# Kernel optimization log

Measured on AMD Instinct MI355X. Metric: run time of the kernel, lower is better.

## Reference

```python
import jax, jax.numpy as jnp
import numpy as np
from jax import lax

B, C, H, W, K = 32, 128, 56, 56, 5
CR = C // 4          # reduced channels in weight-gen MLP
CE = 4 * C           # expanded channels
EPS = 1e-6


def setup_inputs() -> dict:
    key = jax.random.key(0)
    ks = jax.random.split(key, 8)
    s = lambda fan: 1.0 / np.sqrt(fan)
    return {
        "x": jax.random.normal(ks[0], (B, C, H, W), jnp.float32),
        "w_fc1": jax.random.normal(ks[1], (CR, C), jnp.float32) * s(C),
        "ln1_w": jnp.ones((CR,), jnp.float32),
        "ln1_b": jnp.zeros((CR,), jnp.float32),
        "w_fc2": jax.random.normal(ks[2], (C * K * K, CR), jnp.float32) * s(CR),
        "ln2_w": jnp.ones((C,), jnp.float32),
        "ln2_b": jnp.zeros((C,), jnp.float32),
        "w_expand": jax.random.normal(ks[3], (CE, C), jnp.float32) * s(C),
        "w_shrink": jax.random.normal(ks[4], (C, CE), jnp.float32) * s(CE),
        "grn_gamma": jax.random.normal(ks[5], (CE,), jnp.float32) * 0.1,
        "grn_beta": jax.random.normal(ks[6], (CE,), jnp.float32) * 0.1,
    }


def _ln(v, w, b, axis):
    u = v.mean(axis, keepdims=True)
    s2 = jnp.square(v - u).mean(axis, keepdims=True)
    return (v - u) * lax.rsqrt(s2 + EPS) * w + b


def reference(x, w_fc1, ln1_w, ln1_b, w_fc2, ln2_w, ln2_b, w_expand, w_shrink,
              grn_gamma, grn_beta):
    b, c, h, w = x.shape
    # ---- dynamic weight generation: pool -> fc1 -> LN -> fc2 ----
    pooled = x.mean((2, 3))                                  # [B, C]
    hdn = pooled @ w_fc1.T                                   # [B, CR]
    hdn = _ln(hdn, ln1_w, ln1_b, axis=-1)                    # channels_first LN over CR
    dyn = hdn @ w_fc2.T                                      # [B, C*K*K]
    dyn_w = dyn.reshape(b * c, 1, K, K)                      # per-sample depthwise kernels
    # ---- per-sample dynamic depthwise conv (groups = B*C) ----
    pad = K // 2
    out = lax.conv_general_dilated(
        x.reshape(1, b * c, h, w), dyn_w,
        window_strides=(1, 1), padding=[(pad, pad), (pad, pad)],
        dimension_numbers=("NCHW", "OIHW", "NCHW"),
        feature_group_count=b * c,
    ).reshape(b, c, h, w)
    # ---- LN (channels_first) over channel dim ----
    u = out.mean(1, keepdims=True)
    s2 = jnp.square(out - u).mean(1, keepdims=True)
    out = (out - u) * lax.rsqrt(s2 + EPS)
    out = ln2_w[None, :, None, None] * out + ln2_b[None, :, None, None]
    # ---- expand 1x1 -> GELU -> GRN -> shrink 1x1 ----
    out = jnp.einsum("bchw,oc->bohw", out, w_expand)         # [B, 4C, H, W]
    out = jax.nn.gelu(out, approximate=False)
    gx = jnp.sqrt(jnp.sum(jnp.square(out), axis=(2, 3), keepdims=True))  # [B,4C,1,1]
    nx = gx / (gx.mean(1, keepdims=True) + EPS)
    g = grn_gamma[None, :, None, None]
    bt = grn_beta[None, :, None, None]
    out = g * (out * nx) + bt + out
    out = jnp.einsum("bohw,co->bchw", out, w_shrink)         # [B, C, H, W]
    return out + x
```

## Files before the change

kernel.cpp:

```cpp
#include <hip/hip_runtime.h>
#include <hip/hip_bf16.h>

#define B_   32
#define C_   128
#define H_   56
#define W_   56
#define HW_  (H_*W_)
#define BHW_ (B_*HW_)
#define K5_  5
#define KK_  25
#define CR_  32
#define CE_  512
#define EPS_ 1e-6f

typedef __hip_bfloat16 bf16;
typedef __attribute__((ext_vector_type(8))) short short8;
typedef __attribute__((ext_vector_type(4))) float f32x4;


__device__ __forceinline__ float wave_reduce_sum(float v) {
#pragma unroll
  for (int off = 32; off > 0; off >>= 1) v += __shfl_down(v, off, 64);
  return v;
}
__device__ __forceinline__ float bf2f(unsigned short u) {
  return __uint_as_float(((unsigned)u) << 16);
}
__device__ __forceinline__ unsigned short f2bf_bits(float f) {
  bf16 h = __float2bfloat16(f);
  unsigned short u;
  __builtin_memcpy(&u, &h, 2);
  return u;
}
__device__ __forceinline__ float fast_gelu(float v) {
  float t = __expf(-1.702f * v);
  return v * __builtin_amdgcn_rcpf(1.0f + t);
}
__device__ __forceinline__ void glds16(const void* g, void* l) {
  __builtin_amdgcn_global_load_lds(
      (const __attribute__((address_space(1))) unsigned int*)g,
      (__attribute__((address_space(3))) unsigned int*)l, 16, 0, 0);
}

__global__ __launch_bounds__(256) void prep_kernel(const float* __restrict__ we,
                                                   const float* __restrict__ ws,
                                                   const float* __restrict__ beta,
                                                   bf16* __restrict__ weB,
                                                   bf16* __restrict__ wsB,
                                                   float* __restrict__ gx2,
                                                   float* __restrict__ sb) {
  if (blockIdx.x < 576) {
    int i = blockIdx.x * 256 + threadIdx.x;
    if (i < CE_ * C_)          weB[i] = __float2bfloat16(we[i]);
    else if (i < 2 * CE_ * C_) wsB[i - CE_ * C_] = __float2bfloat16(ws[i - CE_ * C_]);
    else                       gx2[i - 2 * CE_ * C_] = 0.f;
  } else {
    int c = blockIdx.x - 576;
    const float* wp = ws + (size_t)c * CE_;
    float acc = 0.f;
    for (int o = threadIdx.x; o < CE_; o += 256) acc += wp[o] * beta[o];
    acc = wave_reduce_sum(acc);
    __shared__ float red[4];
    int lane = threadIdx.x & 63, wid = threadIdx.x >> 6;
    if (lane == 0) red[wid] = acc;
    __syncthreads();
    if (threadIdx.x == 0) sb[c] = red[0] + red[1] + red[2] + red[3];
  }
}

__global__ __launch_bounds__(256) void pool_kernel(const float* __restrict__ x,
                                                   float* __restrict__ pooled) {
  int bc = blockIdx.x;
  const float4* xp4 = reinterpret_cast<const float4*>(x + (size_t)bc * HW_);
  float s = 0.f;
  for (int i = threadIdx.x; i < 784; i += 256) {
    float4 v = xp4[i];
    s += (v.x + v.y) + (v.z + v.w);
  }
  s = wave_reduce_sum(s);
  __shared__ float red[4];
  int lane = threadIdx.x & 63, wid = threadIdx.x >> 6;
  if (lane == 0) red[wid] = s;
  __syncthreads();
  if (threadIdx.x == 0) pooled[bc] = (red[0] + red[1] + red[2] + red[3]) * (1.0f / HW_);
}

__global__ __launch_bounds__(256) void fc_kernel(const float* __restrict__ pooled,
                                                 const float* __restrict__ w_fc1,
                                                 const float* __restrict__ ln1_w,
                                                 const float* __restrict__ ln1_b,
                                                 const float* __restrict__ w_fc2,
                                                 float* __restrict__ dyn) {
  int b = blockIdx.x;
  int tid = threadIdx.x;
  __shared__ float sp[C_];
  __shared__ float sh[CR_];
  __shared__ float shn[CR_];
  __shared__ float stats[2];
  if (tid < C_) sp[tid] = pooled[b * C_ + tid];
  __syncthreads();
  if (tid < CR_) {
    float acc = 0.f;
    const float* wr = w_fc1 + tid * C_;
#pragma unroll 4
    for (int c = 0; c < C_; ++c) acc += sp[c] * wr[c];
    sh[tid] = acc;
  }
  __syncthreads();
  if (tid == 0) {
    float u = 0.f;
    for (int j = 0; j < CR_; ++j) u += sh[j];
    u *= (1.0f / CR_);
    float v = 0.f;
    for (int j = 0; j < CR_; ++j) { float d = sh[j] - u; v += d * d; }
    v *= (1.0f / CR_);
    stats[0] = u;
    stats[1] = rsqrtf(v + EPS_);
  }
  __syncthreads();
  if (tid < CR_) shn[tid] = (sh[tid] - stats[0]) * stats[1] * ln1_w[tid] + ln1_b[tid];
  __syncthreads();
  for (int i = tid; i < C_ * KK_; i += 256) {
    const float* wr = w_fc2 + i * CR_;
    float acc = 0.f;
#pragma unroll
    for (int j = 0; j < CR_; ++j) acc += shn[j] * wr[j];
    dyn[b * (C_ * KK_) + i] = acc;
  }
}

__global__ __launch_bounds__(256) void conv_kernel(const float* __restrict__ x,
                                                   const float* __restrict__ dyn,
                                                   bf16* __restrict__ z) {
  int bc = blockIdx.x;
  int b = bc >> 7;
  int c = bc & 127;
  int tid = threadIdx.x;
  __shared__ float xs[(H_ + 4) * 64];
  __shared__ float wks[KK_];
  {
    int r = tid >> 6;
    int rr = (r < 2) ? r : (56 + r);
    xs[rr * 64 + (tid & 63)] = 0.f;
  }
  if (tid < 224) {
    int r = tid >> 2, q = tid & 3;
    int col = (q < 2) ? q : (56 + q);
    xs[(r + 2) * 64 + col] = 0.f;
  }
  if (tid < KK_) wks[tid] = dyn[b * (C_ * KK_) + c * KK_ + tid];
  const float4* xp4 = reinterpret_cast<const float4*>(x + (size_t)bc * HW_);
  for (int i = tid; i < 784; i += 256) {
    float4 v = xp4[i];
    int h = i / 14, w4 = (i % 14) * 4;
    float* dst = &xs[(h + 2) * 64 + 2 + w4];
    dst[0] = v.x; dst[1] = v.y; dst[2] = v.z; dst[3] = v.w;
  }
  __syncthreads();
  float wr[KK_];
#pragma unroll
  for (int j = 0; j < KK_; ++j) wr[j] = wks[j];
  for (int g = tid; g < 784; g += 256) {
    int h = g / 14;
    int w4 = (g % 14) * 4;
    float a0 = 0.f, a1 = 0.f, a2 = 0.f, a3 = 0.f;
#pragma unroll
    for (int dh = 0; dh < K5_; ++dh) {
      const float* row = &xs[(h + dh) * 64 + w4];
      float4 va = *reinterpret_cast<const float4*>(row);
      float4 vb = *reinterpret_cast<const float4*>(row + 4);
      float v0 = va.x, v1 = va.y, v2 = va.z, v3 = va.w;
      float v4 = vb.x, v5 = vb.y, v6 = vb.z, v7 = vb.w;
      float u0 = wr[dh * 5 + 0], u1 = wr[dh * 5 + 1], u2 = wr[dh * 5 + 2];
      float u3 = wr[dh * 5 + 3], u4 = wr[dh * 5 + 4];
      a0 += v0 * u0 + v1 * u1 + v2 * u2 + v3 * u3 + v4 * u4;
      a1 += v1 * u0 + v2 * u1 + v3 * u2 + v4 * u3 + v5 * u4;
      a2 += v2 * u0 + v3 * u1 + v4 * u2 + v5 * u3 + v6 * u4;
      a3 += v3 * u0 + v4 * u1 + v5 * u2 + v6 * u3 + v7 * u4;
    }
    size_t base = (size_t)bc * HW_ + h * W_ + w4;
    ushort4 pk = make_ushort4(f2bf_bits(a0), f2bf_bits(a1), f2bf_bits(a2), f2bf_bits(a3));
    *reinterpret_cast<ushort4*>(reinterpret_cast<unsigned short*>(z) + base) = pk;
  }
}

__global__ __launch_bounds__(256) void ln_kernel(const bf16* __restrict__ z,
                                                 const float* __restrict__ ln2_w,
                                                 const float* __restrict__ ln2_b,
                                                 bf16* __restrict__ yT) {
  int hw0 = blockIdx.x * 64;
  int b = blockIdx.y;
  int tid = threadIdx.x;
  int wq = tid & 63;
  int cq = tid >> 6;
  __shared__ unsigned short zt[C_][64];
  __shared__ unsigned short yt[64][136];
  __shared__ float redS[4][64];
  __shared__ float redQ[4][64];
  __shared__ float meanArr[64];
  __shared__ float invArr[64];
  const unsigned short* zp = reinterpret_cast<const unsigned short*>(z);
#pragma unroll
  for (int i = 0; i < 4; ++i) {
    int t = tid + 256 * i;
    int c = t >> 3, ch = t & 7;
    int4 v = *reinterpret_cast<const int4*>(zp + ((size_t)(b * C_ + c)) * HW_ + hw0 + ch * 8);
    *reinterpret_cast<int4*>(&zt[c][ch * 8]) = v;
  }
  __syncthreads();
  float s = 0.f, q = 0.f;
#pragma unroll 4
  for (int k = 0; k < 32; ++k) {
    float v = bf2f(zt[cq * 32 + k][wq]);
    s += v;
    q += v * v;
  }
  redS[cq][wq] = s;
  redQ[cq][wq] = q;
  __syncthreads();
  if (cq == 0) {
    float ss = redS[0][wq] + redS[1][wq] + redS[2][wq] + redS[3][wq];
    float qq = redQ[0][wq] + redQ[1][wq] + redQ[2][wq] + redQ[3][wq];
    float m = ss * (1.0f / C_);
    float var = qq * (1.0f / C_) - m * m;
    meanArr[wq] = m;
    invArr[wq] = rsqrtf(fmaxf(var, 0.f) + EPS_);
  }
  __syncthreads();
  float m = meanArr[wq], iv = invArr[wq];
#pragma unroll
  for (int g = 0; g < 4; ++g) {
    unsigned short pk[8];
#pragma unroll
    for (int i = 0; i < 8; ++i) {
      int c = cq * 32 + g * 8 + i;
      float v = bf2f(zt[c][wq]);
      pk[i] = f2bf_bits((v - m) * iv * ln2_w[c] + ln2_b[c]);
    }
    int4 t;
    __builtin_memcpy(&t, pk, 16);
    *reinterpret_cast<int4*>(&yt[wq][cq * 32 + g * 8]) = t;
  }
  __syncthreads();
  unsigned short* yp = reinterpret_cast<unsigned short*>(yT);
#pragma unroll
  for (int i = 0; i < 4; ++i) {
    int t = tid + 256 * i;
    int row = t >> 4, ch = t & 15;
    int4 v = *reinterpret_cast<const int4*>(&yt[row][ch * 8]);
    *reinterpret_cast<int4*>(yp + ((size_t)(b * HW_ + hw0 + row)) * C_ + ch * 8) = v;
  }
}

__global__ __launch_bounds__(256, 4) void gx2_pass(const bf16* __restrict__ yT,
                                                   const bf16* __restrict__ weB,
                                                   float* __restrict__ gx2) {
  int j0 = blockIdx.x * 128;
  int o0 = blockIdx.y * 128;
  int tid = threadIdx.x;
  int lane = tid & 63, wid = tid >> 6;
  int wm = wid >> 1, wn = wid & 1;
  int quad = lane >> 4, l15 = lane & 15;
  __shared__ __align__(16) char smem[32768];
  const short* yS = reinterpret_cast<const short*>(yT);
  const short* weS = reinterpret_cast<const short*>(weB);
  int sr = (wid * 2) * 16 + (lane >> 2);
  int scp = lane & 3;
  auto STAGE = [&](int bs, int k0) {
#pragma unroll
    for (int i = 0; i < 2; ++i) {
      int seg = wid * 2 + i;
      int r = sr + i * 16;
      int c = scp ^ ((r >> 1) & 3);
      char* base = smem + bs * 16384 + seg * 1024;
      glds16(yS + (size_t)(j0 + r) * C_ + k0 + c * 8, base);
      glds16(weS + (size_t)(o0 + r) * C_ + k0 + c * 8, base + 8192);
    }
  };
  f32x4 acc[4][4] = {};
  STAGE(0, 0);
  __syncthreads();
#pragma unroll
  for (int t = 0; t < 4; ++t) {
    if (t < 3) STAGE((t + 1) & 1, (t + 1) * 32);
    const char* ba = smem + (t & 1) * 16384;
    int sx = (quad ^ ((l15 >> 1) & 3)) * 16;
    short8 a[4], bfr[4];
#pragma unroll
    for (int mf = 0; mf < 4; ++mf)
      a[mf] = *reinterpret_cast<const short8*>(ba + (wm * 64 + mf * 16 + l15) * 64 + sx);
#pragma unroll
    for (int nf = 0; nf < 4; ++nf)
      bfr[nf] = *reinterpret_cast<const short8*>(ba + 8192 + (wn * 64 + nf * 16 + l15) * 64 + sx);
#pragma unroll
    for (int mf = 0; mf < 4; ++mf)
#pragma unroll
      for (int nf = 0; nf < 4; ++nf)
        acc[mf][nf] = __builtin_amdgcn_mfma_f32_16x16x32_bf16(a[mf], bfr[nf], acc[mf][nf], 0, 0, 0);
    __syncthreads();
  }
#pragma unroll
  for (int mf = 0; mf < 4; ++mf) {
    int jm = j0 + wm * 64 + mf * 16;
    int bb = jm / HW_;
#pragma unroll
    for (int nf = 0; nf < 4; ++nf) {
      int oc = wn * 64 + nf * 16 + l15;
      float g2 = 0.f;
#pragma unroll
      for (int r = 0; r < 4; ++r) { float ge = fast_gelu(acc[mf][nf][r]); g2 += ge * ge; }
      g2 += __shfl_xor(g2, 16, 64);
      g2 += __shfl_xor(g2, 32, 64);
      if (quad == 0) atomicAdd(&gx2[bb * CE_ + o0 + oc], g2);
    }
  }
}

__global__ __launch_bounds__(512) void grn_scale_kernel(const float* __restrict__ gx2,
                                                        const float* __restrict__ gamma,
                                                        float* __restrict__ scale) {
  int b = blockIdx.x;
  int o = threadIdx.x;
  float gx = sqrtf(gx2[b * CE_ + o]);
  float s = wave_reduce_sum(gx);
  __shared__ float red[8];
  __shared__ float meansh;
  int lane = o & 63, wid = o >> 6;
  if (lane == 0) red[wid] = s;
  __syncthreads();
  if (o == 0) {
    float t = 0.f;
    for (int i = 0; i < 8; ++i) t += red[i];
    meansh = t * (1.0f / CE_);
  }
  __syncthreads();
  scale[b * CE_ + o] = 1.0f + gamma[o] * (gx / (meansh + EPS_));
}

__global__ __launch_bounds__(256, 2) void fused_shrink(const bf16* __restrict__ yT,
                                                       const bf16* __restrict__ weB,
                                                       const bf16* __restrict__ wsB,
                                                       const float* __restrict__ scale,
                                                       const float* __restrict__ sb,
                                                       const float* __restrict__ x,
                                                       float* __restrict__ out) {
  int hw0 = blockIdx.x * 64;
  int b = blockIdx.y;
  int tid = threadIdx.x;
  int lane = tid & 63, wid = tid >> 6;
  int wm = wid >> 1, wn = wid & 1;
  int quad = lane >> 4, l15 = lane & 15;
  __shared__ __align__(16) char smem[66048];
  const short* yS  = reinterpret_cast<const short*>(yT) + (size_t)b * HW_ * C_;
  const short* weS = reinterpret_cast<const short*>(weB);
  const short* wsS = reinterpret_cast<const short*>(wsB);
  const float* scp = scale + b * CE_;
  short (*Es)[132] = reinterpret_cast<short(*)[132]>(smem + 49152);
  int lr4 = lane >> 4;
  int lc16 = lane & 15;
#pragma unroll
  for (int i = 0; i < 4; ++i) {
    int seg = wid * 4 + i;
    int r = seg * 4 + lr4;
    int csrc = lc16 ^ (r & 15);
    glds16(yS + (size_t)(hw0 + r) * C_ + csrc * 8, smem + seg * 1024);
  }
  f32x4 acc2[2][4] = {};
#pragma unroll 1
  for (int n = 0; n < 4; ++n) {
    int oc0 = n * 128;
#pragma unroll
    for (int i = 0; i < 8; ++i) {
      int seg = wid * 8 + i;
      int r = seg * 4 + lr4;
      int csrc = lc16 ^ (r & 15);
      glds16(weS + (size_t)(oc0 + r) * C_ + csrc * 8, smem + 16384 + seg * 1024);
    }
    __syncthreads();
    f32x4 acc1[2][4] = {};
#pragma unroll
    for (int ks = 0; ks < 4; ++ks) {
      short8 a[2], bfr[4];
#pragma unroll
      for (int mf = 0; mf < 2; ++mf) {
        int row = wm * 32 + mf * 16 + l15;
        int cp = (ks * 4 + quad) ^ (row & 15);
        a[mf] = *reinterpret_cast<const short8*>(smem + row * 256 + cp * 16);
      }
#pragma unroll
      for (int nf = 0; nf < 4; ++nf) {
        int row = wn * 64 + nf * 16 + l15;
        int cp = (ks * 4 + quad) ^ (row & 15);
        bfr[nf] = *reinterpret_cast<const short8*>(smem + 16384 + row * 256 + cp * 16);
      }
#pragma unroll
      for (int mf = 0; mf < 2; ++mf)
#pragma unroll
        for (int nf = 0; nf < 4; ++nf)
          acc1[mf][nf] = __builtin_amdgcn_mfma_f32_16x16x32_bf16(a[mf], bfr[nf], acc1[mf][nf], 0, 0, 0);
    }
    __syncthreads();
#pragma unroll
    for (int nf = 0; nf < 4; ++nf) {
      int ocl = wn * 64 + nf * 16 + l15;
      float sc = scp[oc0 + ocl];
#pragma unroll
      for (int mf = 0; mf < 2; ++mf) {
        int jrow = wm * 32 + mf * 16 + quad * 4;
#pragma unroll
        for (int r = 0; r < 4; ++r)
          Es[jrow + r][ocl] = (short)f2bf_bits(fast_gelu(acc1[mf][nf][r]) * sc);
      }
    }
#pragma unroll
    for (int i = 0; i < 8; ++i) {
      int seg = wid * 8 + i;
      int r = seg * 4 + lr4;
      int csrc = lc16 ^ (r & 15);
      glds16(wsS + (size_t)r * CE_ + oc0 + csrc * 8, smem + 16384 + seg * 1024);
    }
    __syncthreads();
#pragma unroll
    for (int ks = 0; ks < 4; ++ks) {
      short8 a2[2], b2[4];
#pragma unroll
      for (int mf = 0; mf < 2; ++mf) {
        int row = wm * 32 + mf * 16 + l15;
        a2[mf] = *reinterpret_cast<const short8*>(
            reinterpret_cast<const char*>(Es) + row * 264 + ks * 64 + quad * 16);
      }
#pragma unroll
      for (int nf = 0; nf < 4; ++nf) {
        int row = wn * 64 + nf * 16 + l15;
        int cp = (ks * 4 + quad) ^ (row & 15);
        b2[nf] = *reinterpret_cast<const short8*>(smem + 16384 + row * 256 + cp * 16);
      }
#pragma unroll
      for (int mf = 0; mf < 2; ++mf)
#pragma unroll
        for (int nf = 0; nf < 4; ++nf)
          acc2[mf][nf] = __builtin_amdgcn_mfma_f32_16x16x32_bf16(a2[mf], b2[nf], acc2[mf][nf], 0, 0, 0);
    }
    __syncthreads();
  }
  float (*Ef)[68] = reinterpret_cast<float(*)[68]>(&smem[0]);
#pragma unroll
  for (int mf = 0; mf < 2; ++mf) {
    int hwr = wm * 32 + mf * 16 + quad * 4;
#pragma unroll
    for (int nf = 0; nf < 4; ++nf)
      *reinterpret_cast<f32x4*>(&Ef[wn * 64 + nf * 16 + l15][hwr]) = acc2[mf][nf];
  }
  __syncthreads();
#pragma unroll
  for (int i = 0; i < 8; ++i) {
    int t = tid + 256 * i;
    int row = t >> 4, ch = t & 15;
    int hw = hw0 + ch * 4;
    size_t base = ((size_t)(b * C_ + row)) * HW_ + hw;
    float add = sb[row];
    f32x4 av = *reinterpret_cast<const f32x4*>(&Ef[row][ch * 4]);
    float4 xv = *reinterpret_cast<const float4*>(x + base);
    float4 ov;
    ov.x = av.x + add + xv.x;
    ov.y = av.y + add + xv.y;
    ov.z = av.z + add + xv.z;
    ov.w = av.w + add + xv.w;
    *reinterpret_cast<float4*>(out + base) = ov;
  }
}

extern "C" void kernel_launch(void* const* d_in, const int* in_sizes, int n_in,
                              void* d_out, int out_size, void* d_ws, size_t ws_size,
                              hipStream_t stream) {
  (void)in_sizes; (void)n_in; (void)out_size; (void)ws_size;
  const float* x        = (const float*)d_in[0];
  const float* w_fc1    = (const float*)d_in[1];
  const float* ln1_w    = (const float*)d_in[2];
  const float* ln1_b    = (const float*)d_in[3];
  const float* w_fc2    = (const float*)d_in[4];
  const float* ln2_w    = (const float*)d_in[5];
  const float* ln2_b    = (const float*)d_in[6];
  const float* w_expand = (const float*)d_in[7];
  const float* w_shrink = (const float*)d_in[8];
  const float* gamma    = (const float*)d_in[9];
  const float* beta     = (const float*)d_in[10];
  float* out = (float*)d_out;

  char* ws = (char*)d_ws;
  float* pooled = (float*)(ws + 0);
  float* dyn    = (float*)(ws + 16384);
  float* gx2    = (float*)(ws + 425984);
  float* scale  = (float*)(ws + 491520);
  float* sb     = (float*)(ws + 557056);
  bf16*  weB    = (bf16*)(ws + 557568);
  bf16*  wsB    = (bf16*)(ws + 688640);
  bf16*  yT     = (bf16*)(ws + 819712);
  bf16*  z      = (bf16*)(ws + 26509824);

  prep_kernel<<<704, 256, 0, stream>>>(w_expand, w_shrink, beta, weB, wsB, gx2, sb);
  pool_kernel<<<B_ * C_, 256, 0, stream>>>(x, pooled);
  fc_kernel<<<B_, 256, 0, stream>>>(pooled, w_fc1, ln1_w, ln1_b, w_fc2, dyn);
  conv_kernel<<<B_ * C_, 256, 0, stream>>>(x, dyn, z);
  ln_kernel<<<dim3(49, B_), 256, 0, stream>>>(z, ln2_w, ln2_b, yT);
  gx2_pass<<<dim3(784, 4), 256, 0, stream>>>(yT, weB, gx2);
  grn_scale_kernel<<<B_, 512, 0, stream>>>(gx2, gamma, scale);
  fused_shrink<<<dim3(49, B_), 256, 0, stream>>>(yT, weB, wsB, scale, sb, x, out);
}
```

Baseline: 278.4 us.

## Merge prep and pool launches; hold yT fragments in registers to raise shrink occupancy

Folds the pool kernel into the weight-prep kernel so both run as one launch. In fused_shrink, the activation A-fragments now load straight from global memory into registers instead of being staged through LDS. The GELU intermediate tile is stored with an XOR swizzle in place of padding. Together these cut LDS from 66 KB to 48 KB and raise launch bounds to 3 blocks per CU, trading higher register pressure for more occupancy.

```diff
diff --git a/kernel.cpp b/kernel.cpp
--- a/kernel.cpp
+++ b/kernel.cpp
@@ -42,20 +42,23 @@
       (__attribute__((address_space(3))) unsigned int*)l, 16, 0, 0);
 }
 
-__global__ __launch_bounds__(256) void prep_kernel(const float* __restrict__ we,
-                                                   const float* __restrict__ ws,
-                                                   const float* __restrict__ beta,
-                                                   bf16* __restrict__ weB,
-                                                   bf16* __restrict__ wsB,
-                                                   float* __restrict__ gx2,
-                                                   float* __restrict__ sb) {
-  if (blockIdx.x < 576) {
-    int i = blockIdx.x * 256 + threadIdx.x;
+__global__ __launch_bounds__(256) void prep_all(const float* __restrict__ we,
+                                                const float* __restrict__ ws,
+                                                const float* __restrict__ beta,
+                                                const float* __restrict__ x,
+                                                bf16* __restrict__ weB,
+                                                bf16* __restrict__ wsB,
+                                                float* __restrict__ gx2,
+                                                float* __restrict__ sb,
+                                                float* __restrict__ pooled) {
+  int bx = blockIdx.x;
+  if (bx < 576) {
+    int i = bx * 256 + threadIdx.x;
     if (i < CE_ * C_)          weB[i] = __float2bfloat16(we[i]);
     else if (i < 2 * CE_ * C_) wsB[i - CE_ * C_] = __float2bfloat16(ws[i - CE_ * C_]);
     else                       gx2[i - 2 * CE_ * C_] = 0.f;
-  } else {
-    int c = blockIdx.x - 576;
+  } else if (bx < 704) {
+    int c = bx - 576;
     const float* wp = ws + (size_t)c * CE_;
     float acc = 0.f;
     for (int o = threadIdx.x; o < CE_; o += 256) acc += wp[o] * beta[o];
@@ -65,24 +68,21 @@
     if (lane == 0) red[wid] = acc;
     __syncthreads();
     if (threadIdx.x == 0) sb[c] = red[0] + red[1] + red[2] + red[3];
-  }
-}
-
-__global__ __launch_bounds__(256) void pool_kernel(const float* __restrict__ x,
-                                                   float* __restrict__ pooled) {
-  int bc = blockIdx.x;
-  const float4* xp4 = reinterpret_cast<const float4*>(x + (size_t)bc * HW_);
-  float s = 0.f;
-  for (int i = threadIdx.x; i < 784; i += 256) {
-    float4 v = xp4[i];
-    s += (v.x + v.y) + (v.z + v.w);
-  }
-  s = wave_reduce_sum(s);
-  __shared__ float red[4];
-  int lane = threadIdx.x & 63, wid = threadIdx.x >> 6;
-  if (lane == 0) red[wid] = s;
-  __syncthreads();
-  if (threadIdx.x == 0) pooled[bc] = (red[0] + red[1] + red[2] + red[3]) * (1.0f / HW_);
+  } else {
+    int bc = bx - 704;
+    const float4* xp4 = reinterpret_cast<const float4*>(x + (size_t)bc * HW_);
+    float s = 0.f;
+    for (int i = threadIdx.x; i < 784; i += 256) {
+      float4 v = xp4[i];
+      s += (v.x + v.y) + (v.z + v.w);
+    }
+    s = wave_reduce_sum(s);
+    __shared__ float redp[4];
+    int lane = threadIdx.x & 63, wid = threadIdx.x >> 6;
+    if (lane == 0) redp[wid] = s;
+    __syncthreads();
+    if (threadIdx.x == 0) pooled[bc] = (redp[0] + redp[1] + redp[2] + redp[3]) * (1.0f / HW_);
+  }
 }
 
 __global__ __launch_bounds__(256) void fc_kernel(const float* __restrict__ pooled,
@@ -337,7 +337,7 @@
   scale[b * CE_ + o] = 1.0f + gamma[o] * (gx / (meansh + EPS_));
 }
 
-__global__ __launch_bounds__(256, 2) void fused_shrink(const bf16* __restrict__ yT,
+__global__ __launch_bounds__(256, 3) void fused_shrink(const bf16* __restrict__ yT,
                                                        const bf16* __restrict__ weB,
                                                        const bf16* __restrict__ wsB,
                                                        const float* __restrict__ scale,
@@ -350,21 +350,21 @@
   int lane = tid & 63, wid = tid >> 6;
   int wm = wid >> 1, wn = wid & 1;
   int quad = lane >> 4, l15 = lane & 15;
-  __shared__ __align__(16) char smem[66048];
+  __shared__ __align__(16) char smem[49152];
   const short* yS  = reinterpret_cast<const short*>(yT) + (size_t)b * HW_ * C_;
   const short* weS = reinterpret_cast<const short*>(weB);
   const short* wsS = reinterpret_cast<const short*>(wsB);
-  const float* scp = scale + b * CE_;
-  short (*Es)[132] = reinterpret_cast<short(*)[132]>(smem + 49152);
+  const float* scl = scale + b * CE_;
+  short8 afr[4][2];
+#pragma unroll
+  for (int ks = 0; ks < 4; ++ks)
+#pragma unroll
+    for (int mf = 0; mf < 2; ++mf)
+      afr[ks][mf] = *reinterpret_cast<const short8*>(
+          yS + (size_t)(hw0 + wm * 32 + mf * 16 + l15) * C_ + ks * 32 + quad * 8);
   int lr4 = lane >> 4;
   int lc16 = lane & 15;
-#pragma unroll
-  for (int i = 0; i < 4; ++i) {
-    int seg = wid * 4 + i;
-    int r = seg * 4 + lr4;
-    int csrc = lc16 ^ (r & 15);
-    glds16(yS + (size_t)(hw0 + r) * C_ + csrc * 8, smem + seg * 1024);
-  }
+  unsigned short* Ep = reinterpret_cast<unsigned short*>(smem + 32768);
   f32x4 acc2[2][4] = {};
 #pragma unroll 1
   for (int n = 0; n < 4; ++n) {
@@ -374,42 +374,40 @@
       int seg = wid * 8 + i;
       int r = seg * 4 + lr4;
       int csrc = lc16 ^ (r & 15);
-      glds16(weS + (size_t)(oc0 + r) * C_ + csrc * 8, smem + 16384 + seg * 1024);
+      glds16(weS + (size_t)(oc0 + r) * C_ + csrc * 8, smem + seg * 1024);
     }
     __syncthreads();
     f32x4 acc1[2][4] = {};
 #pragma unroll
     for (int ks = 0; ks < 4; ++ks) {
-      short8 a[2], bfr[4];
-#pragma unroll
-      for (int mf = 0; mf < 2; ++mf) {
-        int row = wm * 32 + mf * 16 + l15;
-        int cp = (ks * 4 + quad) ^ (row & 15);
-        a[mf] = *reinterpret_cast<const short8*>(smem + row * 256 + cp * 16);
-      }
+      short8 bfr[4];
 #pragma unroll
       for (int nf = 0; nf < 4; ++nf) {
         int row = wn * 64 + nf * 16 + l15;
         int cp = (ks * 4 + quad) ^ (row & 15);
-        bfr[nf] = *reinterpret_cast<const short8*>(smem + 16384 + row * 256 + cp * 16);
+        bfr[nf] = *reinterpret_cast<const short8*>(smem + row * 256 + cp * 16);
       }
 #pragma unroll
       for (int mf = 0; mf < 2; ++mf)
 #pragma unroll
         for (int nf = 0; nf < 4; ++nf)
-          acc1[mf][nf] = __builtin_amdgcn_mfma_f32_16x16x32_bf16(a[mf], bfr[nf], acc1[mf][nf], 0, 0, 0);
+          acc1[mf][nf] = __builtin_amdgcn_mfma_f32_16x16x32_bf16(afr[ks][mf], bfr[nf], acc1[mf][nf], 0, 0, 0);
     }
     __syncthreads();
 #pragma unroll
     for (int nf = 0; nf < 4; ++nf) {
       int ocl = wn * 64 + nf * 16 + l15;
-      float sc = scp[oc0 + ocl];
+      float sc = scl[oc0 + ocl];
+      int lchunk = ocl >> 3, lrem = ocl & 7;
 #pragma unroll
       for (int mf = 0; mf < 2; ++mf) {
-        int jrow = wm * 32 + mf * 16 + quad * 4;
-#pragma unroll
-        for (int r = 0; r < 4; ++r)
-          Es[jrow + r][ocl] = (short)f2bf_bits(fast_gelu(acc1[mf][nf][r]) * sc);
+        int row0 = wm * 32 + mf * 16 + quad * 4;
+#pragma unroll
+        for (int r = 0; r < 4; ++r) {
+          int row = row0 + r;
+          Ep[row * 128 + ((lchunk ^ (row & 15)) << 3) + lrem] =
+              f2bf_bits(fast_gelu(acc1[mf][nf][r]) * sc);
+        }
       }
     }
 #pragma unroll
@@ -417,7 +415,7 @@
       int seg = wid * 8 + i;
       int r = seg * 4 + lr4;
       int csrc = lc16 ^ (r & 15);
-      glds16(wsS + (size_t)r * CE_ + oc0 + csrc * 8, smem + 16384 + seg * 1024);
+      glds16(wsS + (size_t)r * CE_ + oc0 + csrc * 8, smem + seg * 1024);
     }
     __syncthreads();
 #pragma unroll
@@ -426,14 +424,14 @@
 #pragma unroll
       for (int mf = 0; mf < 2; ++mf) {
         int row = wm * 32 + mf * 16 + l15;
-        a2[mf] = *reinterpret_cast<const short8*>(
-            reinterpret_cast<const char*>(Es) + row * 264 + ks * 64 + quad * 16);
+        int cp = (ks * 4 + quad) ^ (row & 15);
+        a2[mf] = *reinterpret_cast<const short8*>(smem + 32768 + row * 256 + cp * 16);
       }
 #pragma unroll
       for (int nf = 0; nf < 4; ++nf) {
         int row = wn * 64 + nf * 16 + l15;
         int cp = (ks * 4 + quad) ^ (row & 15);
-        b2[nf] = *reinterpret_cast<const short8*>(smem + 16384 + row * 256 + cp * 16);
+        b2[nf] = *reinterpret_cast<const short8*>(smem + row * 256 + cp * 16);
       }
 #pragma unroll
       for (int mf = 0; mf < 2; ++mf)
@@ -498,8 +496,7 @@
   bf16*  yT     = (bf16*)(ws + 819712);
   bf16*  z      = (bf16*)(ws + 26509824);
 
-  prep_kernel<<<704, 256, 0, stream>>>(w_expand, w_shrink, beta, weB, wsB, gx2, sb);
-  pool_kernel<<<B_ * C_, 256, 0, stream>>>(x, pooled);
+  prep_all<<<4800, 256, 0, stream>>>(w_expand, w_shrink, beta, x, weB, wsB, gx2, sb, pooled);
   fc_kernel<<<B_, 256, 0, stream>>>(pooled, w_fc1, ln1_w, ln1_b, w_fc2, dyn);
   conv_kernel<<<B_ * C_, 256, 0, stream>>>(x, dyn, z);
   ln_kernel<<<dim3(49, B_), 256, 0, stream>>>(z, ln2_w, ln2_b, yT);
```

After: 304.9 us. +9.5%, slower.
